# Kernel optimization log

Measured on AMD Instinct MI355X. Metric: run time of the kernel, lower is better.

## Reference

```python
import jax, jax.numpy as jnp
import numpy as np

N_NODES = 100000


def gcn_conv(x, edge_index, W, b):
    # PyG GCNConv: add self-loops, symmetric normalization D^-1/2 (A+I) D^-1/2
    src, dst = edge_index[0], edge_index[1]
    n = x.shape[0]
    ones = jnp.ones(src.shape[0], dtype=x.dtype)
    deg = jax.ops.segment_sum(ones, dst, num_segments=n) + 1.0  # +1 self-loop
    dinv = jax.lax.rsqrt(deg)
    h = x @ W  # transform first (smaller gather traffic when out_dim < in_dim)
    norm = dinv[src] * dinv[dst]  # [E]
    msg = h[src] * norm[:, None]  # [E, out]
    agg = jax.ops.segment_sum(msg, dst, num_segments=n)
    agg = agg + h * (dinv * dinv)[:, None]  # self-loop contribution
    return agg + b


def setup_inputs() -> dict:
    key = jax.random.key(0)
    k = jax.random.split(key, 8)
    feature_size = 128
    n_edges = 3200000
    x = jax.random.normal(k[0], (N_NODES, feature_size), dtype=jnp.float32)
    edge_index = jax.random.randint(k[1], (2, n_edges), 0, N_NODES, dtype=jnp.int64)
    # Glorot-ish params
    W1 = jax.random.normal(k[2], (feature_size, 64), dtype=jnp.float32) / np.sqrt(feature_size)
    b1 = jnp.zeros((64,), dtype=jnp.float32)
    W2 = jax.random.normal(k[3], (64, 128), dtype=jnp.float32) / np.sqrt(64)
    b2 = jnp.zeros((128,), dtype=jnp.float32)
    Wfc = jax.random.normal(k[4], (128, 1), dtype=jnp.float32) / np.sqrt(128)
    bfc = jnp.zeros((1,), dtype=jnp.float32)
    return {"x": x, "edge_index": edge_index, "W1": W1, "b1": b1,
            "W2": W2, "b2": b2, "Wfc": Wfc, "bfc": bfc}


def reference(x, edge_index, W1, b1, W2, b2, Wfc, bfc):
    h = jax.nn.relu(gcn_conv(x, edge_index, W1, b1))
    h = jax.nn.relu(gcn_conv(h, edge_index, W2, b2))
    return h @ Wfc + bfc  # [N, 1]
```

## Files before the change

### kernel.cpp

```cpp
#include <hip/hip_runtime.h>
#include <hip/hip_fp16.h>

#define NN 100000
#define NBIN 256
#define RANGE 391
#define CAP 16384
#define CAPL 16384

__device__ __forceinline__ void gemm1_tile(char* smem, int tile,
                                           const float* __restrict__ X,
                                           const float* __restrict__ W,
                                           __half* __restrict__ H, int n, int t) {
    constexpr int K = 128, C = 64, RPT = 2, CG = 16, RT = 64, XS = K + 4;
    float* Ws = (float*)smem;
    float* Xs = (float*)(smem + 32768);

    for (int i = t * 4; i < K * C; i += 2048)
        *(float4*)&Ws[i] = *(const float4*)&W[i];

    const int row0 = tile * RT;
    for (int i = t * 4; i < RT * K; i += 2048) {
        int r = i / K, k = i % K;
        int gr = row0 + r;
        float4 v = make_float4(0.f, 0.f, 0.f, 0.f);
        if (gr < n) v = *(const float4*)&X[(long long)gr * K + k];
        *(float4*)&Xs[r * XS + k] = v;
    }
    __syncthreads();

    const int cg = t % CG, rs = t / CG;
    float acc[RPT][4];
#pragma unroll
    for (int i = 0; i < RPT; ++i)
#pragma unroll
        for (int j = 0; j < 4; ++j) acc[i][j] = 0.f;

#pragma unroll 2
    for (int k4 = 0; k4 < K / 4; ++k4) {
        float4 xv[RPT];
#pragma unroll
        for (int i = 0; i < RPT; ++i)
            xv[i] = *(float4*)&Xs[(rs * RPT + i) * XS + k4 * 4];
#pragma unroll
        for (int j = 0; j < 4; ++j) {
            float4 w = *(float4*)&Ws[(k4 * 4 + j) * C + cg * 4];
#pragma unroll
            for (int i = 0; i < RPT; ++i) {
                float xvj = (&xv[i].x)[j];
                acc[i][0] = fmaf(xvj, w.x, acc[i][0]);
                acc[i][1] = fmaf(xvj, w.y, acc[i][1]);
                acc[i][2] = fmaf(xvj, w.z, acc[i][2]);
                acc[i][3] = fmaf(xvj, w.w, acc[i][3]);
            }
        }
    }
#pragma unroll
    for (int i = 0; i < RPT; ++i) {
        int gr = row0 + rs * RPT + i;
        if (gr < n) {
            union { __half h[4]; uint2 u; } pk;
            pk.h[0] = __float2half(acc[i][0]);
            pk.h[1] = __float2half(acc[i][1]);
            pk.h[2] = __float2half(acc[i][2]);
            pk.h[3] = __float2half(acc[i][3]);
            *(uint2*)&H[(long long)gr * C + cg * 4] = pk.u;
        }
    }
}

__global__ __launch_bounds__(512) void k_binA_gemm1(
        const int* __restrict__ ei_lo, int E,
        int* __restrict__ g_bincnt, unsigned* __restrict__ binbuf,
        const float* __restrict__ X, const float* __restrict__ W1,
        __half* __restrict__ H, int n, int nBA) {
    __shared__ alignas(16) char smem[66560];
    const int t = threadIdx.x;
    const int b = blockIdx.x;
    const bool isBin = ((b & 1) == 0) && ((b >> 1) < nBA);
    if (isBin) {
        const int blk = b >> 1;
        int* cnt   = (int*)smem;
        int* basep = (int*)(smem + 1024);
        int* pos   = (int*)(smem + 2048);
        int* pis64 = (int*)(smem + 3072);
        if (t < NBIN) { cnt[t] = 0; pos[t] = 0; }
        if (t == 0) {
            const unsigned* u = (const unsigned*)ei_lo;
            int is64 = 1;
            for (int i = 0; i < 64; ++i)
                if (u[2 * i + 1] != 0u) { is64 = 0; break; }
            *pis64 = is64;
        }
        __syncthreads();
        const int s = (*pis64) ? 2 : 1;
        constexpr int ITER = 8;
        const int base = blk * (512 * ITER);
        unsigned pk[ITER];
        int bn[ITER];
#pragma unroll
        for (int i = 0; i < ITER; ++i) {
            int e = base + i * 512 + t;
            if (e < E) {
                int src = __builtin_nontemporal_load(&ei_lo[(long long)s * e]);
                int dst = __builtin_nontemporal_load(&ei_lo[(long long)s * (E + e)]);
                int bb = dst / RANGE;
                bn[i] = bb;
                pk[i] = ((unsigned)(dst - bb * RANGE) << 17) | (unsigned)src;
                atomicAdd(&cnt[bb], 1);
            } else bn[i] = -1;
        }
        __syncthreads();
        if (t < NBIN) basep[t] = atomicAdd(&g_bincnt[t], cnt[t]);
        __syncthreads();
#pragma unroll
        for (int i = 0; i < ITER; ++i) {
            if (bn[i] >= 0) {
                int r = atomicAdd(&pos[bn[i]], 1);
                binbuf[(long long)bn[i] * CAP + basep[bn[i]] + r] = pk[i];
            }
        }
    } else {
        gemm1_tile(smem, b >> 1, X, W1, H, n, t);
    }
}

__global__ __launch_bounds__(512) void k_build_gemm1(
        const unsigned* __restrict__ binbuf, const int* __restrict__ g_bincnt,
        int* __restrict__ row_ptr, float* __restrict__ dinv, int* __restrict__ csr,
        int n, int E,
        const float* __restrict__ X, const float* __restrict__ W1,
        __half* __restrict__ H, int tile0) {
    __shared__ alignas(16) char smem[69632];
    const int t = threadIdx.x;
    if ((int)blockIdx.x < NBIN) {
        unsigned* ebuf = (unsigned*)smem;
        int* cnt  = (int*)(smem + 65536);
        int* ssum = (int*)(smem + 67584);
        int* pref = (int*)(smem + 68608);
        const int bin = blockIdx.x;
        const int lo = bin * RANGE;
        const int rn = min(RANGE, n - lo);
        const int nE = min(g_bincnt[bin], CAPL);
        const unsigned* __restrict__ src = binbuf + (long long)bin * CAP;

        cnt[t] = 0;
        if (t < NBIN) pref[t] = g_bincnt[t];
        __syncthreads();

        for (int i = t; i < nE; i += 512) {
            unsigned e = src[i];
            ebuf[i] = e;
            atomicAdd(&cnt[(int)(e >> 17)], 1);
        }
        __syncthreads();

        for (int off = 1; off < NBIN; off <<= 1) {
            int add = (t >= off && t < NBIN) ? pref[t - off] : 0;
            __syncthreads();
            if (t < NBIN) pref[t] += add;
            __syncthreads();
        }
        const int bstart = (bin > 0) ? pref[bin - 1] : 0;

        int a = 0, bcnt = 0;
        if (t < 256) { a = cnt[2 * t]; bcnt = cnt[2 * t + 1]; ssum[t] = a + bcnt; }
        __syncthreads();
        for (int off = 1; off < 256; off <<= 1) {
            int add = (t >= off && t < 256) ? ssum[t - off] : 0;
            __syncthreads();
            if (t < 256) ssum[t] += add;
            __syncthreads();
        }
        if (t < 256) {
            int prev = (t > 0) ? ssum[t - 1] : 0;
            cnt[2 * t] = prev;
            cnt[2 * t + 1] = prev + a;
            if (2 * t < rn) {
                row_ptr[lo + 2 * t] = bstart + prev;
                dinv[lo + 2 * t] = rsqrtf((float)a + 1.f);
            }
            if (2 * t + 1 < rn) {
                row_ptr[lo + 2 * t + 1] = bstart + prev + a;
                dinv[lo + 2 * t + 1] = rsqrtf((float)bcnt + 1.f);
            }
        }
        if (bin == NBIN - 1 && t == 0) row_ptr[n] = E;
        __syncthreads();

        for (int i = t; i < nE; i += 512) {
            unsigned e = ebuf[i];
            int slot = bstart + atomicAdd(&cnt[(int)(e >> 17)], 1);
            csr[slot] = (int)(e & 0x1FFFFu);
        }
    } else {
        gemm1_tile(smem, tile0 + ((int)blockIdx.x - NBIN), X, W1, H, n, t);
    }
}

__global__ __launch_bounds__(256) void k_scale(__half* __restrict__ h,
                                               const float* __restrict__ dinv, int n8) {
    int idx = blockIdx.x * 256 + threadIdx.x;
    if (idx >= n8) return;
    float d = dinv[idx >> 3];
    uint4 u = *(uint4*)&h[(long long)idx * 8];
    union { __half hh[8]; uint4 u; } o;
    float2 f;
    f = __half22float2(*(__half2*)&u.x); o.hh[0] = __float2half(f.x * d); o.hh[1] = __float2half(f.y * d);
    f = __half22float2(*(__half2*)&u.y); o.hh[2] = __float2half(f.x * d); o.hh[3] = __float2half(f.y * d);
    f = __half22float2(*(__half2*)&u.z); o.hh[4] = __float2half(f.x * d); o.hh[5] = __float2half(f.y * d);
    f = __half22float2(*(__half2*)&u.w); o.hh[6] = __float2half(f.x * d); o.hh[7] = __float2half(f.y * d);
    *(uint4*)&h[(long long)idx * 8] = o.u;
}

template <bool RELU>
__global__ __launch_bounds__(256) void k_gather(const __half* __restrict__ h,
                                                const int* __restrict__ row_ptr,
                                                const int* __restrict__ csr,
                                                const float* __restrict__ dinv,
                                                const float* __restrict__ bias,
                                                __half* __restrict__ out, int n) {
    const int node = blockIdx.x * 4 + (threadIdx.x >> 6);
    if (node >= n) return;
    const int lane = threadIdx.x & 63;
    const int g = lane >> 3;
    const int fl = lane & 7;
    const float d = dinv[node];
    const int beg = row_ptr[node], end = row_ptr[node + 1];

    uint4 su = make_uint4(0u, 0u, 0u, 0u);
    if (g == 0) su = *(const uint4*)&h[(long long)node * 64 + fl * 8];

    __half2 z = __float2half2_rn(0.f);
    __half2 acc0 = z, acc1 = z, acc2 = z, acc3 = z;

    const int nfull = (end - beg) >> 4;
    int i = beg;
    for (int it = 0; it < nfull; ++it, i += 16) {
        int s0 = csr[i + g];
        int s1 = csr[i + 8 + g];
        uint4 u0 = *(const uint4*)&h[(long long)s0 * 64 + fl * 8];
        uint4 u1 = *(const uint4*)&h[(long long)s1 * 64 + fl * 8];
        __half2 p0 = __hadd2(*(__half2*)&u0.x, *(__half2*)&u1.x);
        __half2 p1 = __hadd2(*(__half2*)&u0.y, *(__half2*)&u1.y);
        __half2 p2 = __hadd2(*(__half2*)&u0.z, *(__half2*)&u1.z);
        __half2 p3 = __hadd2(*(__half2*)&u0.w, *(__half2*)&u1.w);
        acc0 = __hadd2(acc0, p0);
        acc1 = __hadd2(acc1, p1);
        acc2 = __hadd2(acc2, p2);
        acc3 = __hadd2(acc3, p3);
    }
    if (i + g < end) {
        int s0 = csr[i + g];
        uint4 u0 = *(const uint4*)&h[(long long)s0 * 64 + fl * 8];
        acc0 = __hadd2(acc0, *(__half2*)&u0.x);
        acc1 = __hadd2(acc1, *(__half2*)&u0.y);
        acc2 = __hadd2(acc2, *(__half2*)&u0.z);
        acc3 = __hadd2(acc3, *(__half2*)&u0.w);
    }
    if (i + 8 + g < end) {
        int s1 = csr[i + 8 + g];
        uint4 u1 = *(const uint4*)&h[(long long)s1 * 64 + fl * 8];
        acc0 = __hadd2(acc0, *(__half2*)&u1.x);
        acc1 = __hadd2(acc1, *(__half2*)&u1.y);
        acc2 = __hadd2(acc2, *(__half2*)&u1.z);
        acc3 = __hadd2(acc3, *(__half2*)&u1.w);
    }

    float2 f0 = __half22float2(acc0);
    float2 f1 = __half22float2(acc1);
    float2 f2 = __half22float2(acc2);
    float2 f3 = __half22float2(acc3);
    float r0 = f0.x, r1 = f0.y, r2 = f1.x, r3 = f1.y;
    float r4 = f2.x, r5 = f2.y, r6 = f3.x, r7 = f3.y;
#pragma unroll
    for (int off = 8; off <= 32; off <<= 1) {
        r0 += __shfl_xor(r0, off, 64);
        r1 += __shfl_xor(r1, off, 64);
        r2 += __shfl_xor(r2, off, 64);
        r3 += __shfl_xor(r3, off, 64);
        r4 += __shfl_xor(r4, off, 64);
        r5 += __shfl_xor(r5, off, 64);
        r6 += __shfl_xor(r6, off, 64);
        r7 += __shfl_xor(r7, off, 64);
    }
    if (g == 0) {
        float2 s0 = __half22float2(*(__half2*)&su.x);
        float2 s1 = __half22float2(*(__half2*)&su.y);
        float2 s2 = __half22float2(*(__half2*)&su.z);
        float2 s3 = __half22float2(*(__half2*)&su.w);
        r0 += s0.x; r1 += s0.y; r2 += s1.x; r3 += s1.y;
        r4 += s2.x; r5 += s2.y; r6 += s3.x; r7 += s3.y;
        union { __half hh[8]; uint4 u; } o;
        if (RELU) {
            float4 bv0 = *(const float4*)&bias[fl * 8];
            float4 bv1 = *(const float4*)&bias[fl * 8 + 4];
            o.hh[0] = __float2half(fmaxf(fmaf(d, r0, bv0.x), 0.f) * d);
            o.hh[1] = __float2half(fmaxf(fmaf(d, r1, bv0.y), 0.f) * d);
            o.hh[2] = __float2half(fmaxf(fmaf(d, r2, bv0.z), 0.f) * d);
            o.hh[3] = __float2half(fmaxf(fmaf(d, r3, bv0.w), 0.f) * d);
            o.hh[4] = __float2half(fmaxf(fmaf(d, r4, bv1.x), 0.f) * d);
            o.hh[5] = __float2half(fmaxf(fmaf(d, r5, bv1.y), 0.f) * d);
            o.hh[6] = __float2half(fmaxf(fmaf(d, r6, bv1.z), 0.f) * d);
            o.hh[7] = __float2half(fmaxf(fmaf(d, r7, bv1.w), 0.f) * d);
        } else {
            o.hh[0] = __float2half(d * r0);
            o.hh[1] = __float2half(d * r1);
            o.hh[2] = __float2half(d * r2);
            o.hh[3] = __float2half(d * r3);
            o.hh[4] = __float2half(d * r4);
            o.hh[5] = __float2half(d * r5);
            o.hh[6] = __float2half(d * r6);
            o.hh[7] = __float2half(d * r7);
        }
        *(uint4*)&out[(long long)node * 64 + fl * 8] = o.u;
    }
}

__global__ __launch_bounds__(256) void k_gemm2fc(const __half* __restrict__ G,
                                                 const float* __restrict__ W2,
                                                 const float* __restrict__ b2,
                                                 const float* __restrict__ Wfc,
                                                 const float* __restrict__ bfc,
                                                 float* __restrict__ out, int n) {
    constexpr int K = 64, C = 128, CG = 32, RPT = 4, RT = 32, XS = K + 4;
    __shared__ float Ws[K * C];
    __shared__ float Xs[RT * XS];
    const int t = threadIdx.x;

    for (int i = t * 4; i < K * C; i += 1024)
        *(float4*)&Ws[i] = *(const float4*)&W2[i];

    const int row0 = blockIdx.x * RT;
    for (int i = t * 4; i < RT * K; i += 1024) {
        int r = i / K, k = i % K;
        int gr = row0 + r;
        float4 v = make_float4(0.f, 0.f, 0.f, 0.f);
        if (gr < n) {
            uint2 u = *(const uint2*)&G[(long long)gr * K + k];
            float2 f0 = __half22float2(*(__half2*)&u.x);
            float2 f1 = __half22float2(*(__half2*)&u.y);
            v = make_float4(f0.x, f0.y, f1.x, f1.y);
        }
        *(float4*)&Xs[r * XS + k] = v;
    }
    __syncthreads();

    const int cg = t % CG, rs = t / CG;
    float acc[RPT][4];
#pragma unroll
    for (int i = 0; i < RPT; ++i)
#pragma unroll
        for (int j = 0; j < 4; ++j) acc[i][j] = 0.f;

#pragma unroll 2
    for (int k4 = 0; k4 < K / 4; ++k4) {
        float4 xv[RPT];
#pragma unroll
        for (int i = 0; i < RPT; ++i)
            xv[i] = *(float4*)&Xs[(rs * RPT + i) * XS + k4 * 4];
#pragma unroll
        for (int j = 0; j < 4; ++j) {
            float4 w = *(float4*)&Ws[(k4 * 4 + j) * C + cg * 4];
#pragma unroll
            for (int i = 0; i < RPT; ++i) {
                float xvj = (&xv[i].x)[j];
                acc[i][0] = fmaf(xvj, w.x, acc[i][0]);
                acc[i][1] = fmaf(xvj, w.y, acc[i][1]);
                acc[i][2] = fmaf(xvj, w.z, acc[i][2]);
                acc[i][3] = fmaf(xvj, w.w, acc[i][3]);
            }
        }
    }

    float4 bv = *(const float4*)&b2[cg * 4];
    float4 wf = *(const float4*)&Wfc[cg * 4];
#pragma unroll
    for (int i = 0; i < RPT; ++i) {
        float p = fmaxf(acc[i][0] + bv.x, 0.f) * wf.x
                + fmaxf(acc[i][1] + bv.y, 0.f) * wf.y
                + fmaxf(acc[i][2] + bv.z, 0.f) * wf.z
                + fmaxf(acc[i][3] + bv.w, 0.f) * wf.w;
#pragma unroll
        for (int off = 16; off; off >>= 1) p += __shfl_down(p, off, 32);
        int gr = row0 + rs * RPT + i;
        if (cg == 0 && gr < n) out[gr] = p + bfc[0];
    }
}

extern "C" void kernel_launch(void* const* d_in, const int* in_sizes, int n_in,
                              void* d_out, int out_size, void* d_ws, size_t ws_size,
                              hipStream_t stream) {
    const float* x   = (const float*)d_in[0];
    const void*  ei  = d_in[1];
    const float* W1  = (const float*)d_in[2];
    const float* b1  = (const float*)d_in[3];
    const float* W2  = (const float*)d_in[4];
    const float* b2  = (const float*)d_in[5];
    const float* Wfc = (const float*)d_in[6];
    const float* bfc = (const float*)d_in[7];
    float* out = (float*)d_out;

    const int N = NN;
    const int E = in_sizes[1] / 2;

    char* ws = (char*)d_ws;
    size_t o = 0;
    auto carve = [&](size_t bytes) {
        char* p = ws + o;
        o = (o + bytes + 255) & ~(size_t)255;
        return p;
    };
    float*    dinv      = (float*)carve((size_t)N * 4);
    int*      row_ptr   = (int*)carve((size_t)(N + 1) * 4);
    int*      g_bincnt  = (int*)carve((size_t)NBIN * 4);
    int*      csr       = (int*)carve((size_t)E * 4);
    unsigned* binbuf    = (unsigned*)carve((size_t)NBIN * CAP * 4);
    __half*   bufA      = (__half*)carve((size_t)N * 64 * 2);
    __half*   bufB      = (__half*)carve((size_t)N * 64 * 2);
    __half*   bufG      = (__half*)carve((size_t)N * 64 * 2);

    const int* ei_lo = (const int*)ei;

    const int BA    = (E + 4095) / 4096;
    const int TILES = (N + 63) / 64;
    const int T1    = (BA - 1 < TILES) ? (BA - 1) : TILES;

    hipMemsetAsync(g_bincnt, 0, (size_t)NBIN * 4, stream);
    k_binA_gemm1<<<BA + T1, 512, 0, stream>>>(ei_lo, E, g_bincnt, binbuf,
                                              x, W1, bufA, N, BA);
    k_build_gemm1<<<NBIN + (TILES - T1), 512, 0, stream>>>(binbuf, g_bincnt,
                                                           row_ptr, dinv, csr, N, E,
                                                           x, W1, bufA, T1);
    k_scale<<<(N * 8 + 255) / 256, 256, 0, stream>>>(bufA, dinv, N * 8);

    k_gather<true><<<(N + 3) / 4, 256, 0, stream>>>(bufA, row_ptr, csr, dinv, b1, bufB, N);
    k_gather<false><<<(N + 3) / 4, 256, 0, stream>>>(bufB, row_ptr, csr, dinv, nullptr, bufG, N);
    k_gemm2fc<<<(N + 31) / 32, 256, 0, stream>>>(bufG, W2, b2, Wfc, bfc, out, N);
}
```

Baseline: 237.2 us.

## Use MFMA fp16 for gemm2+fc and double edges per binning block

Rewrites the final GEMM+ReLU+FC kernel to use 16x16x32 fp16 MFMA instructions, with W2 transposed into shared memory as fp16 and each wave handling 16 rows. This replaces the fp32 FMA loop and the fp32 staging of activations. Separately, the binning kernel now processes 16 edges per thread instead of 8, which halves the number of binning blocks and the global atomics on bin counters. W2 is now rounded to fp16, which adds some precision loss, and fewer binning blocks also reduce how many GEMM1 tiles can overlap in the first kernel.

```diff
diff --git a/kernel.cpp b/kernel.cpp
--- a/kernel.cpp
+++ b/kernel.cpp
@@ -6,6 +6,9 @@
 #define RANGE 391
 #define CAP 16384
 #define CAPL 16384
+
+typedef _Float16 f16x8 __attribute__((ext_vector_type(8)));
+typedef float f32x4 __attribute__((ext_vector_type(4)));
 
 __device__ __forceinline__ void gemm1_tile(char* smem, int tile,
                                            const float* __restrict__ X,
@@ -93,7 +96,7 @@
         }
         __syncthreads();
         const int s = (*pis64) ? 2 : 1;
-        constexpr int ITER = 8;
+        constexpr int ITER = 16;
         const int base = blk * (512 * ITER);
         unsigned pk[ITER];
         int bn[ITER];
@@ -322,68 +325,59 @@
                                                  const float* __restrict__ Wfc,
                                                  const float* __restrict__ bfc,
                                                  float* __restrict__ out, int n) {
-    constexpr int K = 64, C = 128, CG = 32, RPT = 4, RT = 32, XS = K + 4;
-    __shared__ float Ws[K * C];
-    __shared__ float Xs[RT * XS];
+    __shared__ __align__(16) _Float16 W2T[128][72];
+    __shared__ float b2s[128], wfs[128];
     const int t = threadIdx.x;
-
-    for (int i = t * 4; i < K * C; i += 1024)
-        *(float4*)&Ws[i] = *(const float4*)&W2[i];
-
-    const int row0 = blockIdx.x * RT;
-    for (int i = t * 4; i < RT * K; i += 1024) {
-        int r = i / K, k = i % K;
-        int gr = row0 + r;
-        float4 v = make_float4(0.f, 0.f, 0.f, 0.f);
-        if (gr < n) {
-            uint2 u = *(const uint2*)&G[(long long)gr * K + k];
-            float2 f0 = __half22float2(*(__half2*)&u.x);
-            float2 f1 = __half22float2(*(__half2*)&u.y);
-            v = make_float4(f0.x, f0.y, f1.x, f1.y);
-        }
-        *(float4*)&Xs[r * XS + k] = v;
-    }
+    for (int i = t; i < 64 * 128; i += 256) {
+        int k = i >> 7, c = i & 127;
+        W2T[c][k] = (_Float16)W2[i];
+    }
+    if (t < 128) { b2s[t] = b2[t]; wfs[t] = Wfc[t]; }
     __syncthreads();
 
-    const int cg = t % CG, rs = t / CG;
-    float acc[RPT][4];
-#pragma unroll
-    for (int i = 0; i < RPT; ++i)
-#pragma unroll
-        for (int j = 0; j < 4; ++j) acc[i][j] = 0.f;
-
-#pragma unroll 2
-    for (int k4 = 0; k4 < K / 4; ++k4) {
-        float4 xv[RPT];
-#pragma unroll
-        for (int i = 0; i < RPT; ++i)
-            xv[i] = *(float4*)&Xs[(rs * RPT + i) * XS + k4 * 4];
-#pragma unroll
-        for (int j = 0; j < 4; ++j) {
-            float4 w = *(float4*)&Ws[(k4 * 4 + j) * C + cg * 4];
-#pragma unroll
-            for (int i = 0; i < RPT; ++i) {
-                float xvj = (&xv[i].x)[j];
-                acc[i][0] = fmaf(xvj, w.x, acc[i][0]);
-                acc[i][1] = fmaf(xvj, w.y, acc[i][1]);
-                acc[i][2] = fmaf(xvj, w.z, acc[i][2]);
-                acc[i][3] = fmaf(xvj, w.w, acc[i][3]);
-            }
-        }
-    }
-
-    float4 bv = *(const float4*)&b2[cg * 4];
-    float4 wf = *(const float4*)&Wfc[cg * 4];
-#pragma unroll
-    for (int i = 0; i < RPT; ++i) {
-        float p = fmaxf(acc[i][0] + bv.x, 0.f) * wf.x
-                + fmaxf(acc[i][1] + bv.y, 0.f) * wf.y
-                + fmaxf(acc[i][2] + bv.z, 0.f) * wf.z
-                + fmaxf(acc[i][3] + bv.w, 0.f) * wf.w;
-#pragma unroll
-        for (int off = 16; off; off >>= 1) p += __shfl_down(p, off, 32);
-        int gr = row0 + rs * RPT + i;
-        if (cg == 0 && gr < n) out[gr] = p + bfc[0];
+    const int w = t >> 6;
+    const int l = t & 63;
+    const int c16 = l & 15;
+    const int q = l >> 4;
+    const int row0 = blockIdx.x * 64 + w * 16;
+    const int ar = row0 + c16;
+
+    const _Float16* Gf = (const _Float16*)G;
+    f16x8 a0 = {}, a1 = {};
+    if (ar < n) {
+        a0 = *(const f16x8*)&Gf[(long long)ar * 64 + q * 8];
+        a1 = *(const f16x8*)&Gf[(long long)ar * 64 + 32 + q * 8];
+    }
+
+    float p0 = 0.f, p1 = 0.f, p2 = 0.f, p3 = 0.f;
+#pragma unroll
+    for (int ct = 0; ct < 8; ++ct) {
+        f16x8 b0 = *(const f16x8*)&W2T[ct * 16 + c16][q * 8];
+        f16x8 b1 = *(const f16x8*)&W2T[ct * 16 + c16][32 + q * 8];
+        f32x4 acc = {0.f, 0.f, 0.f, 0.f};
+        acc = __builtin_amdgcn_mfma_f32_16x16x32_f16(a0, b0, acc, 0, 0, 0);
+        acc = __builtin_amdgcn_mfma_f32_16x16x32_f16(a1, b1, acc, 0, 0, 0);
+        int col = ct * 16 + c16;
+        float bb = b2s[col], wf = wfs[col];
+        p0 += fmaxf(acc[0] + bb, 0.f) * wf;
+        p1 += fmaxf(acc[1] + bb, 0.f) * wf;
+        p2 += fmaxf(acc[2] + bb, 0.f) * wf;
+        p3 += fmaxf(acc[3] + bb, 0.f) * wf;
+    }
+#pragma unroll
+    for (int off = 1; off <= 8; off <<= 1) {
+        p0 += __shfl_xor(p0, off, 64);
+        p1 += __shfl_xor(p1, off, 64);
+        p2 += __shfl_xor(p2, off, 64);
+        p3 += __shfl_xor(p3, off, 64);
+    }
+    if (c16 == 0) {
+        int row = row0 + q * 4;
+        float bf = bfc[0];
+        if (row < n)     out[row]     = p0 + bf;
+        if (row + 1 < n) out[row + 1] = p1 + bf;
+        if (row + 2 < n) out[row + 2] = p2 + bf;
+        if (row + 3 < n) out[row + 3] = p3 + bf;
     }
 }
 
@@ -421,7 +415,7 @@
 
     const int* ei_lo = (const int*)ei;
 
-    const int BA    = (E + 4095) / 4096;
+    const int BA    = (E + 8191) / 8192;
     const int TILES = (N + 63) / 64;
     const int T1    = (BA - 1 < TILES) ? (BA - 1) : TILES;
 
@@ -435,5 +429,5 @@
 
     k_gather<true><<<(N + 3) / 4, 256, 0, stream>>>(bufA, row_ptr, csr, dinv, b1, bufB, N);
     k_gather<false><<<(N + 3) / 4, 256, 0, stream>>>(bufB, row_ptr, csr, dinv, nullptr, bufG, N);
-    k_gemm2fc<<<(N + 31) / 32, 256, 0, stream>>>(bufG, W2, b2, Wfc, bfc, out, N);
-}
+    k_gemm2fc<<<(N + 63) / 64, 256, 0, stream>>>(bufG, W2, b2, Wfc, bfc, out, N);
+}
```

Measured after the change: 223.3 us. -5.9%, faster.
